# Performance work log

Measured on AMD Instinct MI355X. Metric: run time of the kernel, lower is better.

## Reference

```python
import jax, jax.numpy as jnp
import numpy as np

B, V, L, D, H, W = 4, 2, 8192, 768, 12, 512  # batch, views, seq, d_model, heads, window


def _layernorm(x, g, b, eps=1e-5):
    # matches torch LayerNorm computed in fp32 then cast back
    x32 = x.astype(jnp.float32)
    m = x32.mean(-1, keepdims=True)
    v = ((x32 - m) ** 2).mean(-1, keepdims=True)
    return ((x32 - m) * jax.lax.rsqrt(v + eps) * g + b).astype(x.dtype)


def _mha(q_in, k_in, v_in, wqkv, bqkv, wo, bo, h):
    # torch nn.MultiheadAttention (eval mode, no mask). inputs [..., S, d]
    d = q_in.shape[-1]
    hd = d // h
    scale = 1.0 / np.sqrt(hd)
    q = (q_in @ wqkv[:d].T + bqkv[:d]).reshape(*q_in.shape[:-1], h, hd)
    k = (k_in @ wqkv[d:2 * d].T + bqkv[d:2 * d]).reshape(*k_in.shape[:-1], h, hd)
    v = (v_in @ wqkv[2 * d:].T + bqkv[2 * d:]).reshape(*v_in.shape[:-1], h, hd)
    scores = jnp.einsum('...qhd,...khd->...hqk', q, k) * scale
    a = jax.nn.softmax(scores, axis=-1)
    o = jnp.einsum('...hqk,...khd->...qhd', a, v).reshape(q_in.shape)
    return o @ wo.T + bo


def reference(x, ln1_g, ln1_b, ln2_g, ln2_b,
              a1_wqkv, a1_bqkv, a1_wo, a1_bo,
              a2_wqkv, a2_bqkv, a2_wo, a2_bo,
              fc_w, fc_b, proj_w, proj_b, index):
    b, v, l, c = x.shape
    y = _layernorm(x, ln1_g, ln1_b)
    shifted = (index % 2 == 1)  # index is a static Python int
    xs = jnp.roll(x, W // 2, axis=2) if shifted else x
    p = l // W
    xw = xs.reshape(b, v, p, W, c)  # window partition (only x is rolled, as in source)
    yw = y.reshape(b, v, p, W, c)
    # cross-view windowed attention: Q=norm view i, K=norm view j, V=raw view i
    v1 = _mha(yw[:, 0], yw[:, 1], xw[:, 0], a1_wqkv, a1_bqkv, a1_wo, a1_bo, H)
    v2 = _mha(yw[:, 1], yw[:, 0], xw[:, 1], a2_wqkv, a2_bqkv, a2_wo, a2_bo, H)
    att = jnp.stack([v1, v2], axis=1).reshape(b, v, l, c)
    if shifted:
        att = jnp.roll(att, -(W // 2), axis=2)
    x = x + att
    y2 = _layernorm(x, ln2_g, ln2_b)
    h = y2 @ fc_w.T + fc_b
    h = h * jax.nn.sigmoid(1.702 * h)  # fast GELU
    return x + (h @ proj_w.T + proj_b)


def setup_inputs() -> dict:
    key = jax.random.key(0)
    ks = jax.random.split(key, 10)
    s = 0.02
    return {
        'x': jax.random.normal(ks[0], (B, V, L, D), jnp.float32),
        'ln1_g': jnp.ones((D,), jnp.float32),
        'ln1_b': jnp.zeros((D,), jnp.float32),
        'ln2_g': jnp.ones((D,), jnp.float32),
        'ln2_b': jnp.zeros((D,), jnp.float32),
        'a1_wqkv': jax.random.normal(ks[1], (3 * D, D), jnp.float32) * s,
        'a1_bqkv': jnp.zeros((3 * D,), jnp.float32),
        'a1_wo': jax.random.normal(ks[2], (D, D), jnp.float32) * s,
        'a1_bo': jnp.zeros((D,), jnp.float32),
        'a2_wqkv': jax.random.normal(ks[3], (3 * D, D), jnp.float32) * s,
        'a2_bqkv': jnp.zeros((3 * D,), jnp.float32),
        'a2_wo': jax.random.normal(ks[4], (D, D), jnp.float32) * s,
        'a2_bo': jnp.zeros((D,), jnp.float32),
        'fc_w': jax.random.normal(ks[5], (4 * D, D), jnp.float32) * s,
        'fc_b': jnp.zeros((4 * D,), jnp.float32),
        'proj_w': jax.random.normal(ks[6], (D, 4 * D), jnp.float32) * s,
        'proj_b': jnp.zeros((D,), jnp.float32),
        'index': 0,
    }
```

## Files before the change

kernel.cpp:

```cpp
#include <hip/hip_runtime.h>
#include <hip/hip_bf16.h>

typedef __bf16 bf16x8 __attribute__((ext_vector_type(8)));
typedef float  f32x4  __attribute__((ext_vector_type(4)));
typedef short  s16x4  __attribute__((ext_vector_type(4)));
typedef unsigned short u16;

#define L2E 1.44269504088896f
#define SBAR  __builtin_amdgcn_s_barrier()
#define SCHED __builtin_amdgcn_sched_barrier(0)

static __device__ __forceinline__ u16 f2bf(float f) {
  unsigned u = __builtin_bit_cast(unsigned, f);
  u += 0x7fffu + ((u >> 16) & 1u);
  return (u16)(u >> 16);
}

static __device__ __forceinline__ void gld_lds16(const void* g, void* l) {
  __builtin_amdgcn_global_load_lds((const __attribute__((address_space(1))) unsigned*)g,
                                   (__attribute__((address_space(3))) unsigned*)l, 16, 0, 0);
}

__global__ __launch_bounds__(256)
void cvtk(const float* __restrict__ s, u16* __restrict__ d, int n) {
  const int i = (blockIdx.x * 256 + threadIdx.x) * 4;
  if (i >= n) return;
  const float4 f = *(const float4*)(s + i);
  s16x4 p;
  p[0] = (short)f2bf(f.x); p[1] = (short)f2bf(f.y);
  p[2] = (short)f2bf(f.z); p[3] = (short)f2bf(f.w);
  *(s16x4*)(d + i) = p;
}

__global__ __launch_bounds__(256)
void lnk(const float* __restrict__ x, const float* __restrict__ gw,
         const float* __restrict__ bw, u16* __restrict__ y,
         u16* __restrict__ xv, int viewmajor) {
  const int lane = threadIdx.x & 63;
  const int tok = blockIdx.x * 4 + (threadIdx.x >> 6);
  const float* xr = x + (size_t)tok * 768;
  float4 v[3];
  float s = 0.f, sq = 0.f;
#pragma unroll
  for (int j = 0; j < 3; ++j) {
    v[j] = *(const float4*)(xr + j * 256 + lane * 4);
    s  += v[j].x + v[j].y + v[j].z + v[j].w;
    sq += v[j].x * v[j].x + v[j].y * v[j].y + v[j].z * v[j].z + v[j].w * v[j].w;
  }
#pragma unroll
  for (int o = 1; o < 64; o <<= 1) { s += __shfl_xor(s, o); sq += __shfl_xor(sq, o); }
  const float mean = s * (1.f / 768.f);
  const float var  = sq * (1.f / 768.f) - mean * mean;
  const float rstd = rsqrtf(var + 1e-5f);
  size_t yrow = (size_t)tok;
  if (viewmajor) {
    const int b_ = tok >> 14, vv = (tok >> 13) & 1, l_ = tok & 8191;
    yrow = ((size_t)((vv << 2) + b_) << 13) + l_;
  }
#pragma unroll
  for (int j = 0; j < 3; ++j) {
    const float4 g4 = *(const float4*)(gw + j * 256 + lane * 4);
    const float4 b4 = *(const float4*)(bw + j * 256 + lane * 4);
    s16x4 py;
    py[0] = (short)f2bf((v[j].x - mean) * rstd * g4.x + b4.x);
    py[1] = (short)f2bf((v[j].y - mean) * rstd * g4.y + b4.y);
    py[2] = (short)f2bf((v[j].z - mean) * rstd * g4.z + b4.z);
    py[3] = (short)f2bf((v[j].w - mean) * rstd * g4.w + b4.w);
    *(s16x4*)(y + yrow * 768 + j * 256 + lane * 4) = py;
    if (xv) {
      s16x4 px;
      px[0] = (short)f2bf(v[j].x); px[1] = (short)f2bf(v[j].y);
      px[2] = (short)f2bf(v[j].z); px[3] = (short)f2bf(v[j].w);
      *(s16x4*)(xv + yrow * 768 + j * 256 + lane * 4) = px;
    }
  }
}

template<int MODE>
__global__ __launch_bounds__(512, 2)
void gemm_bt(const u16* __restrict__ A, const u16* __restrict__ B,
             const float* __restrict__ bias, void* __restrict__ Cp,
             int N, int K,
             const float* __restrict__ xres, const int* __restrict__ idxp,
             int vview) {
  __shared__ char lds[131072];
  const int t = threadIdx.x;
  const int lane = t & 63;
  const int wid = t >> 6;
  const int wm = wid >> 2, wn = wid & 3;

  const int cpx = gridDim.x >> 3;
  const int bid = (blockIdx.x & 7) * cpx + (blockIdx.x >> 3);
  const int Ntiles = N >> 8;
  const int PPB = Ntiles << 3;
  const int panel = bid / PPB;
  const int rem = bid - panel * PPB;
  const int nt = rem >> 3;
  const int mt = (panel << 3) + (rem & 7);

  const int urow = t >> 3;
  const int koff = ((t & 7) ^ (urow & 7)) << 3;
  const u16* Asrc = A + (size_t)(mt * 256 + urow) * K + koff;
  const u16* Bsrc = B + (size_t)(nt * 256 + urow) * K + koff;
  const int wdst = wid << 10;

  auto stgA = [&](int d, int kt, int u0) {
    char* base = (char*)lds + d * 32768 + wdst;
    gld_lds16(Asrc + (size_t)(u0 * 64) * K + kt * 64, base + u0 * 8192);
    gld_lds16(Asrc + (size_t)(u0 * 64 + 64) * K + kt * 64, base + u0 * 8192 + 8192);
  };
  auto stgB = [&](int d, int kt, int u0) {
    char* base = (char*)lds + 65536 + d * 32768 + wdst;
    gld_lds16(Bsrc + (size_t)(u0 * 64) * K + kt * 64, base + u0 * 8192);
    gld_lds16(Bsrc + (size_t)(u0 * 64 + 64) * K + kt * 64, base + u0 * 8192 + 8192);
  };

  const int c15 = lane & 15, g = lane >> 4;
  const int axor = c15 & 7;
  const char* LAb = (char*)lds + (wm * 128 + c15) * 128;
  const char* LBb = (char*)lds + 65536 + (wn * 64 + c15) * 128;
  bf16x8 av[4][2], bv[4][2];
  auto rdA = [&](int d, int mh) {
#pragma unroll
    for (int m = 0; m < 4; ++m)
#pragma unroll
      for (int ks = 0; ks < 2; ++ks)
        av[m][ks] = *(const bf16x8*)(LAb + d * 32768 + (mh * 64 + m * 16) * 128 +
                                     (((ks << 2) | g) ^ axor) * 16);
  };
  auto rdB = [&](int d) {
#pragma unroll
    for (int n = 0; n < 4; ++n)
#pragma unroll
      for (int ks = 0; ks < 2; ++ks)
        bv[n][ks] = *(const bf16x8*)(LBb + d * 32768 + (n * 16) * 128 +
                                     (((ks << 2) | g) ^ axor) * 16);
  };

  f32x4 acc[8][4] = {};
  auto QD = [&](int mh, int nh) {
    __builtin_amdgcn_s_setprio(1);
#pragma unroll
    for (int ks = 0; ks < 2; ++ks)
#pragma unroll
      for (int m = 0; m < 4; ++m)
#pragma unroll
        for (int n = 0; n < 2; ++n)
          acc[mh * 4 + m][nh * 2 + n] = __builtin_amdgcn_mfma_f32_16x16x32_bf16(
              av[m][ks], bv[nh * 2 + n][ks], acc[mh * 4 + m][nh * 2 + n], 0, 0, 0);
    __builtin_amdgcn_s_setprio(0);
  };

  const int nk = K >> 6, niter = nk >> 1, last = nk - 1;

  stgA(0, 0, 0); stgA(0, 0, 2); stgB(0, 0, 0); stgB(0, 0, 2);
  stgB(1, 1, 0); stgB(1, 1, 2); stgA(1, 1, 0);
  asm volatile("s_waitcnt vmcnt(6)" ::: "memory");
  SBAR; SCHED;

  for (int it = 0; it < niter; ++it) {
    const int i2 = it * 2;
    const int t1 = (i2 + 1 < nk) ? i2 + 1 : last;
    const int t2 = (i2 + 2 < nk) ? i2 + 2 : last;
    const int t3 = (i2 + 3 < nk) ? i2 + 3 : last;

    rdA(0, 0); rdB(0); stgA(1, t1, 2);
    SCHED; SBAR; SCHED; QD(0, 0); SCHED; SBAR; SCHED;
    stgB(0, t2, 0);
    SCHED; SBAR; SCHED; QD(0, 1); SCHED; SBAR; SCHED;
    rdA(0, 1); stgB(0, t2, 2);
    SCHED; SBAR; SCHED; QD(1, 1); SCHED; SBAR; SCHED;
    stgA(0, t2, 0);
    asm volatile("s_waitcnt vmcnt(6)" ::: "memory");
    SCHED; SBAR; SCHED; QD(1, 0); SCHED; SBAR; SCHED;
    rdA(1, 0); rdB(1); stgA(0, t2, 2);
    SCHED; SBAR; SCHED; QD(0, 0); SCHED; SBAR; SCHED;
    stgB(1, t3, 0);
    SCHED; SBAR; SCHED; QD(0, 1); SCHED; SBAR; SCHED;
    rdA(1, 1); stgB(1, t3, 2);
    SCHED; SBAR; SCHED; QD(1, 1); SCHED; SBAR; SCHED;
    stgA(1, t3, 0);
    asm volatile("s_waitcnt vmcnt(6)" ::: "memory");
    SCHED; SBAR; SCHED; QD(1, 0); SCHED; SBAR; SCHED;
  }

  int shift = 0;
  if constexpr (MODE == 2) shift = (idxp[0] & 1) ? 256 : 0;

  const int rb0 = mt * 256 + wm * 128 + (g << 2);
  const int cbase = nt * 256 + wn * 64 + c15;
#pragma unroll
  for (int mi = 0; mi < 8; ++mi) {
    const int row = rb0 + mi * 16;
#pragma unroll
    for (int nj = 0; nj < 4; ++nj) {
      const int col = cbase + nj * 16;
      const float bvv = bias[col];
      if constexpr (MODE == 0) {
        u16* C = (u16*)Cp;
#pragma unroll
        for (int r = 0; r < 4; ++r)
          C[(size_t)(row + r) * N + col] = f2bf(acc[mi][nj][r] + bvv);
      } else if constexpr (MODE == 1) {
        u16* C = (u16*)Cp;
        const int hh = col >> 6, dd = col & 63;
        const int b_ = row >> 13, l_ = row & 8191;
        s16x4 pk;
#pragma unroll
        for (int r = 0; r < 4; ++r) pk[r] = (short)f2bf(acc[mi][nj][r] + bvv);
        *(s16x4*)(C + (((size_t)((b_ * 12 + hh) << 6) + dd) << 13) + l_) = pk;
      } else if constexpr (MODE == 2) {
        float* C = (float*)Cp;
        const int b_ = row >> 13, p_ = row & 8191;
        const int l0 = (p_ - shift) & 8191;
        const size_t rbase = ((size_t)((b_ << 1) + vview) << 13) + l0;
#pragma unroll
        for (int r = 0; r < 4; ++r) {
          const size_t idx = (rbase + r) * 768 + col;
          C[idx] = xres[idx] + acc[mi][nj][r] + bvv;
        }
      } else if constexpr (MODE == 3) {
        u16* C = (u16*)Cp;
#pragma unroll
        for (int r = 0; r < 4; ++r) {
          const float u = acc[mi][nj][r] + bvv;
          const float e = __builtin_amdgcn_exp2f(-2.45546693f * u);
          C[(size_t)(row + r) * N + col] = f2bf(u / (1.f + e));
        }
      } else {
        float* C = (float*)Cp;
#pragma unroll
        for (int r = 0; r < 4; ++r) {
          const size_t idx = (size_t)(row + r) * 768 + col;
          C[idx] = C[idx] + acc[mi][nj][r] + bvv;
        }
      }
    }
  }
}

__global__ __launch_bounds__(512, 2)
void attnk(const u16* __restrict__ Q1, const u16* __restrict__ K1, const u16* __restrict__ V1,
           const u16* __restrict__ Q2, const u16* __restrict__ K2, const u16* __restrict__ V2,
           u16* __restrict__ O, const int* __restrict__ idxp) {
  __shared__ char lds[131072];
  const int t = threadIdx.x;
  const int lane = t & 63;
  const int c = lane & 15, g = lane >> 4;
  const int wid = t >> 6;
  int bb = blockIdx.x;
  const int h = bb % 12; bb /= 12;
  const int w = bb & 15; bb >>= 4;
  const int b = bb & 3;
  const int a = bb >> 2;
  const int shift = (idxp[0] & 1) ? 256 : 0;

  const u16* Q  = a ? Q2 : Q1;
  const u16* Kb = a ? K2 : K1;
  const u16* Vt = a ? V2 : V1;
  const int kbase = b * 8192 + w * 512;
  const u16* Vts = Vt + ((size_t)(b * 12 + h) << 19);

  const int qrow0 = b * 8192 + w * 512 + wid * 64;
  bf16x8 qf[4][2];
#pragma unroll
  for (int q = 0; q < 4; ++q)
#pragma unroll
    for (int hf = 0; hf < 2; ++hf)
      qf[q][hf] = *(const bf16x8*)(Q + (size_t)(qrow0 + q * 16 + c) * 768 + h * 64 + hf * 32 + g * 8);

  {
    const int r0 = t >> 3, ch = t & 7;
    char* kdst = (char*)lds + (wid << 10);
#pragma unroll
    for (int p = 0; p < 8; ++p) {
      const int row = p * 64 + r0;
      gld_lds16(Kb + (size_t)(kbase + row) * 768 + h * 64 + ((ch ^ (row & 7)) << 3),
                kdst + p * 8192);
    }
    char* vdst = (char*)lds + 65536 + (wid << 10);
#pragma unroll
    for (int p = 0; p < 8; ++p) {
      const int vrow = p * 8 + wid;
      const int cg = lane ^ (vrow & 7);
      const int l = (w * 512 + cg * 8 - shift) & 8191;
      gld_lds16(Vts + (size_t)vrow * 8192 + l, vdst + p * 8192);
    }
  }
  __syncthreads();

  f32x4 oacc[4][4] = {};
  f32x4 psum[4] = {};
  const float CEXP = 0.125f * L2E;
  const char* LK = (char*)lds;
  const char* LV = (char*)lds + 65536;

  for (int kt = 0; kt < 32; ++kt) {
    const int krow = kt * 16 + c;
    const int ksw = krow & 7;
    const bf16x8 kf0 = *(const bf16x8*)(LK + krow * 128 + ((g ^ ksw) << 4));
    const bf16x8 kf1 = *(const bf16x8*)(LK + krow * 128 + (((4 | g) ^ ksw) << 4));
    s16x4 vf[4];
#pragma unroll
    for (int df = 0; df < 4; ++df) {
      const int vr = df * 16 + c;
      vf[df] = *(const s16x4*)(LV + vr * 1024 +
                               (((kt * 2 + (g >> 1)) ^ (vr & 7)) << 4) + ((g & 1) << 3));
    }

    const f32x4 z = {0.f, 0.f, 0.f, 0.f};
    s16x4 pk[4];
#pragma unroll
    for (int q = 0; q < 4; ++q) {
      f32x4 sc2 = __builtin_amdgcn_mfma_f32_16x16x32_bf16(kf0, qf[q][0], z, 0, 0, 0);
      sc2 = __builtin_amdgcn_mfma_f32_16x16x32_bf16(kf1, qf[q][1], sc2, 0, 0, 0);
      f32x4 pv;
      pv[0] = __builtin_amdgcn_exp2f(sc2[0] * CEXP);
      pv[1] = __builtin_amdgcn_exp2f(sc2[1] * CEXP);
      pv[2] = __builtin_amdgcn_exp2f(sc2[2] * CEXP);
      pv[3] = __builtin_amdgcn_exp2f(sc2[3] * CEXP);
      psum[q] += pv;
      pk[q][0] = (short)f2bf(pv[0]);
      pk[q][1] = (short)f2bf(pv[1]);
      pk[q][2] = (short)f2bf(pv[2]);
      pk[q][3] = (short)f2bf(pv[3]);
    }
#pragma unroll
    for (int df = 0; df < 4; ++df)
#pragma unroll
      for (int q = 0; q < 4; ++q)
        oacc[df][q] = __builtin_amdgcn_mfma_f32_16x16x16bf16_1k(vf[df], pk[q], oacc[df][q], 0, 0, 0);
  }

  const size_t orow0 = (size_t)(a * 32768 + qrow0);
#pragma unroll
  for (int q = 0; q < 4; ++q) {
    float ss = psum[q][0] + psum[q][1] + psum[q][2] + psum[q][3];
    ss += __shfl_xor(ss, 16);
    ss += __shfl_xor(ss, 32);
    const float inv = 1.f / ss;
#pragma unroll
    for (int df = 0; df < 4; ++df) {
      s16x4 po;
#pragma unroll
      for (int r = 0; r < 4; ++r) po[r] = (short)f2bf(oacc[df][q][r] * inv);
      *(s16x4*)(O + (orow0 + q * 16 + c) * 768 + h * 64 + df * 16 + g * 4) = po;
    }
  }
}

extern "C" void kernel_launch(void* const* d_in, const int* in_sizes, int n_in,
                              void* d_out, int out_size, void* d_ws, size_t ws_size,
                              hipStream_t stream) {
  const float* x       = (const float*)d_in[0];
  const float* ln1_g   = (const float*)d_in[1];
  const float* ln1_b   = (const float*)d_in[2];
  const float* ln2_g   = (const float*)d_in[3];
  const float* ln2_b   = (const float*)d_in[4];
  const float* a1_wqkv = (const float*)d_in[5];
  const float* a1_bqkv = (const float*)d_in[6];
  const float* a1_wo   = (const float*)d_in[7];
  const float* a1_bo   = (const float*)d_in[8];
  const float* a2_wqkv = (const float*)d_in[9];
  const float* a2_bqkv = (const float*)d_in[10];
  const float* a2_wo   = (const float*)d_in[11];
  const float* a2_bo   = (const float*)d_in[12];
  const float* fc_w    = (const float*)d_in[13];
  const float* fc_b    = (const float*)d_in[14];
  const float* proj_w  = (const float*)d_in[15];
  const float* proj_b  = (const float*)d_in[16];
  const int*   idxp    = (const int*)d_in[17];
  float* out = (float*)d_out;

  u16* p = (u16*)d_ws;
  u16* w1  = p; p += (size_t)2304 * 768;
  u16* w2  = p; p += (size_t)2304 * 768;
  u16* wo1 = p; p += (size_t)768 * 768;
  u16* wo2 = p; p += (size_t)768 * 768;
  u16* fcw = p; p += (size_t)3072 * 768;
  u16* pjw = p; p += (size_t)768 * 3072;
  u16* y   = p; p += (size_t)65536 * 768;
  u16* xv  = p; p += (size_t)65536 * 768;
  u16* Q1  = p; p += (size_t)32768 * 768;
  u16* K1  = p; p += (size_t)32768 * 768;
  u16* V1  = p; p += (size_t)32768 * 768;
  u16* Q2  = p; p += (size_t)32768 * 768;
  u16* K2  = p; p += (size_t)32768 * 768;
  u16* V2  = p; p += (size_t)32768 * 768;
  u16* Ob  = p; p += (size_t)65536 * 768;
  u16* hb  = Q1;

  cvtk<<<1728, 256, 0, stream>>>(a1_wqkv, w1, 2304 * 768);
  cvtk<<<1728, 256, 0, stream>>>(a2_wqkv, w2, 2304 * 768);
  cvtk<<<576,  256, 0, stream>>>(a1_wo, wo1, 768 * 768);
  cvtk<<<576,  256, 0, stream>>>(a2_wo, wo2, 768 * 768);
  cvtk<<<2304, 256, 0, stream>>>(fc_w, fcw, 3072 * 768);
  cvtk<<<2304, 256, 0, stream>>>(proj_w, pjw, 768 * 3072);

  lnk<<<16384, 256, 0, stream>>>(x, ln1_g, ln1_b, y, xv, 1);

  const size_t VS = (size_t)32768 * 768;
  gemm_bt<0><<<384, 512, 0, stream>>>(y,        w1,                  a1_bqkv,        Q1, 768, 768, nullptr, nullptr, 0);
  gemm_bt<0><<<384, 512, 0, stream>>>(y + VS,   w1 + 768 * 768,      a1_bqkv + 768,  K1, 768, 768, nullptr, nullptr, 0);
  gemm_bt<1><<<384, 512, 0, stream>>>(xv,       w1 + 2 * 768 * 768,  a1_bqkv + 1536, V1, 768, 768, nullptr, nullptr, 0);
  gemm_bt<0><<<384, 512, 0, stream>>>(y + VS,   w2,                  a2_bqkv,        Q2, 768, 768, nullptr, nullptr, 0);
  gemm_bt<0><<<384, 512, 0, stream>>>(y,        w2 + 768 * 768,      a2_bqkv + 768,  K2, 768, 768, nullptr, nullptr, 0);
  gemm_bt<1><<<384, 512, 0, stream>>>(xv + VS,  w2 + 2 * 768 * 768,  a2_bqkv + 1536, V2, 768, 768, nullptr, nullptr, 0);

  attnk<<<1536, 512, 0, stream>>>(Q1, K1, V1, Q2, K2, V2, Ob, idxp);

  gemm_bt<2><<<384, 512, 0, stream>>>(Ob,      wo1, a1_bo, out, 768, 768, x, idxp, 0);
  gemm_bt<2><<<384, 512, 0, stream>>>(Ob + VS, wo2, a2_bo, out, 768, 768, x, idxp, 1);

  lnk<<<16384, 256, 0, stream>>>(out, ln2_g, ln2_b, y, nullptr, 0);

  gemm_bt<3><<<3072, 512, 0, stream>>>(y, fcw, fc_b, hb, 3072, 768, nullptr, nullptr, 0);

  gemm_bt<4><<<768, 512, 0, stream>>>(hb, pjw, proj_b, out, 768, 3072, nullptr, nullptr, 0);
}
```

Measured before the change: 1.502 ms.

## Replace 256x256 8-wave GEMM with 256x128 4-wave grouped GEMM kernel

Replaces the templated 256x256-tile, 512-thread GEMM and its hand-interleaved 8-phase schedule with a 256x128-tile, 256-thread kernel. The new kernel uses a simple double-buffered K=32 loop and a smaller LDS footprint so more blocks can be resident. Several GEMMs are batched into a single grouped launch through an argument struct: the six QKV projections in one, the two output projections in another. The epilogue mode becomes a runtime branch instead of a template parameter. This trades the tuned fine-grained MFMA/load interleaving and larger-tile reuse for fewer launches and higher occupancy, at the cost of more barriers per unit of work.

```diff
diff --git a/kernel.cpp b/kernel.cpp
--- a/kernel.cpp
+++ b/kernel.cpp
@@ -7,7 +7,6 @@
 typedef unsigned short u16;
 
 #define L2E 1.44269504088896f
-#define SBAR  __builtin_amdgcn_s_barrier()
 #define SCHED __builtin_amdgcn_sched_barrier(0)
 
 static __device__ __forceinline__ u16 f2bf(float f) {
@@ -76,119 +75,106 @@
   }
 }
 
-template<int MODE>
-__global__ __launch_bounds__(512, 2)
-void gemm_bt(const u16* __restrict__ A, const u16* __restrict__ B,
-             const float* __restrict__ bias, void* __restrict__ Cp,
-             int N, int K,
-             const float* __restrict__ xres, const int* __restrict__ idxp,
-             int vview) {
-  __shared__ char lds[131072];
+struct GArgs {
+  const u16* A[6]; const u16* B[6]; const float* bias[6]; void* C[6];
+  int mode[6]; int vv[6];
+  int bps, N, K;
+  const float* xres; const int* idxp;
+};
+
+__global__ __launch_bounds__(256, 2)
+void gemmk(GArgs ga) {
+  __shared__ char lds[49152];
   const int t = threadIdx.x;
   const int lane = t & 63;
   const int wid = t >> 6;
-  const int wm = wid >> 2, wn = wid & 3;
-
-  const int cpx = gridDim.x >> 3;
-  const int bid = (blockIdx.x & 7) * cpx + (blockIdx.x >> 3);
-  const int Ntiles = N >> 8;
+  const int wm = wid >> 1, wn = wid & 1;
+
+  const int sub = blockIdx.x / ga.bps;
+  const int local = blockIdx.x - sub * ga.bps;
+  const u16* A = ga.A[sub];
+  const u16* B = ga.B[sub];
+  const float* bias = ga.bias[sub];
+  void* Cp = ga.C[sub];
+  const int mode = ga.mode[sub];
+  const int vview = ga.vv[sub];
+  const int N = ga.N, K = ga.K;
+
+  const int cpx = ga.bps >> 3;
+  const int bid = (local & 7) * cpx + (local >> 3);
+  const int Ntiles = N >> 7;
   const int PPB = Ntiles << 3;
   const int panel = bid / PPB;
   const int rem = bid - panel * PPB;
   const int nt = rem >> 3;
   const int mt = (panel << 3) + (rem & 7);
 
-  const int urow = t >> 3;
-  const int koff = ((t & 7) ^ (urow & 7)) << 3;
-  const u16* Asrc = A + (size_t)(mt * 256 + urow) * K + koff;
-  const u16* Bsrc = B + (size_t)(nt * 256 + urow) * K + koff;
+  const int r0 = t >> 2;
+  const int csrc = (t & 3) ^ ((r0 >> 1) & 3);
+  const u16* Asrc = A + (size_t)(mt * 256 + r0) * K + csrc * 8;
+  const u16* Bsrc = B + (size_t)(nt * 128 + r0) * K + csrc * 8;
   const int wdst = wid << 10;
 
-  auto stgA = [&](int d, int kt, int u0) {
-    char* base = (char*)lds + d * 32768 + wdst;
-    gld_lds16(Asrc + (size_t)(u0 * 64) * K + kt * 64, base + u0 * 8192);
-    gld_lds16(Asrc + (size_t)(u0 * 64 + 64) * K + kt * 64, base + u0 * 8192 + 8192);
+  auto stage = [&](int d, int kt) {
+#pragma unroll
+    for (int i = 0; i < 4; ++i)
+      gld_lds16(Asrc + (size_t)(i * 64) * K + kt * 32,
+                (char*)lds + d * 16384 + i * 4096 + wdst);
+#pragma unroll
+    for (int i = 0; i < 2; ++i)
+      gld_lds16(Bsrc + (size_t)(i * 64) * K + kt * 32,
+                (char*)lds + 32768 + d * 8192 + i * 4096 + wdst);
   };
-  auto stgB = [&](int d, int kt, int u0) {
-    char* base = (char*)lds + 65536 + d * 32768 + wdst;
-    gld_lds16(Bsrc + (size_t)(u0 * 64) * K + kt * 64, base + u0 * 8192);
-    gld_lds16(Bsrc + (size_t)(u0 * 64 + 64) * K + kt * 64, base + u0 * 8192 + 8192);
-  };
 
   const int c15 = lane & 15, g = lane >> 4;
-  const int axor = c15 & 7;
-  const char* LAb = (char*)lds + (wm * 128 + c15) * 128;
-  const char* LBb = (char*)lds + 65536 + (wn * 64 + c15) * 128;
-  bf16x8 av[4][2], bv[4][2];
-  auto rdA = [&](int d, int mh) {
-#pragma unroll
-    for (int m = 0; m < 4; ++m)
-#pragma unroll
-      for (int ks = 0; ks < 2; ++ks)
-        av[m][ks] = *(const bf16x8*)(LAb + d * 32768 + (mh * 64 + m * 16) * 128 +
-                                     (((ks << 2) | g) ^ axor) * 16);
+  bf16x8 av[8], bv[4];
+  auto rdA = [&](int d) {
+#pragma unroll
+    for (int m = 0; m < 8; ++m) {
+      const int row = wm * 128 + m * 16 + c15;
+      av[m] = *(const bf16x8*)((char*)lds + d * 16384 + row * 64 +
+                               ((g ^ ((row >> 1) & 3)) << 4));
+    }
   };
   auto rdB = [&](int d) {
 #pragma unroll
-    for (int n = 0; n < 4; ++n)
-#pragma unroll
-      for (int ks = 0; ks < 2; ++ks)
-        bv[n][ks] = *(const bf16x8*)(LBb + d * 32768 + (n * 16) * 128 +
-                                     (((ks << 2) | g) ^ axor) * 16);
+    for (int n = 0; n < 4; ++n) {
+      const int row = wn * 64 + n * 16 + c15;
+      bv[n] = *(const bf16x8*)((char*)lds + 32768 + d * 8192 + row * 64 +
+                               ((g ^ ((row >> 1) & 3)) << 4));
+    }
   };
 
   f32x4 acc[8][4] = {};
-  auto QD = [&](int mh, int nh) {
+  const int nk = K >> 5;
+
+  stage(0, 0);
+#pragma unroll 2
+  for (int kt = 0; kt < nk; ++kt) {
+    const int d = kt & 1;
+    if (kt + 1 < nk) {
+      stage(d ^ 1, kt + 1);
+      asm volatile("s_waitcnt vmcnt(6)" ::: "memory");
+    } else {
+      asm volatile("s_waitcnt vmcnt(0)" ::: "memory");
+    }
+    __builtin_amdgcn_s_barrier();
+    SCHED;
+    rdA(d); rdB(d);
     __builtin_amdgcn_s_setprio(1);
 #pragma unroll
-    for (int ks = 0; ks < 2; ++ks)
-#pragma unroll
-      for (int m = 0; m < 4; ++m)
-#pragma unroll
-        for (int n = 0; n < 2; ++n)
-          acc[mh * 4 + m][nh * 2 + n] = __builtin_amdgcn_mfma_f32_16x16x32_bf16(
-              av[m][ks], bv[nh * 2 + n][ks], acc[mh * 4 + m][nh * 2 + n], 0, 0, 0);
+    for (int m = 0; m < 8; ++m)
+#pragma unroll
+      for (int n = 0; n < 4; ++n)
+        acc[m][n] = __builtin_amdgcn_mfma_f32_16x16x32_bf16(av[m], bv[n], acc[m][n], 0, 0, 0);
     __builtin_amdgcn_s_setprio(0);
-  };
-
-  const int nk = K >> 6, niter = nk >> 1, last = nk - 1;
-
-  stgA(0, 0, 0); stgA(0, 0, 2); stgB(0, 0, 0); stgB(0, 0, 2);
-  stgB(1, 1, 0); stgB(1, 1, 2); stgA(1, 1, 0);
-  asm volatile("s_waitcnt vmcnt(6)" ::: "memory");
-  SBAR; SCHED;
-
-  for (int it = 0; it < niter; ++it) {
-    const int i2 = it * 2;
-    const int t1 = (i2 + 1 < nk) ? i2 + 1 : last;
-    const int t2 = (i2 + 2 < nk) ? i2 + 2 : last;
-    const int t3 = (i2 + 3 < nk) ? i2 + 3 : last;
-
-    rdA(0, 0); rdB(0); stgA(1, t1, 2);
-    SCHED; SBAR; SCHED; QD(0, 0); SCHED; SBAR; SCHED;
-    stgB(0, t2, 0);
-    SCHED; SBAR; SCHED; QD(0, 1); SCHED; SBAR; SCHED;
-    rdA(0, 1); stgB(0, t2, 2);
-    SCHED; SBAR; SCHED; QD(1, 1); SCHED; SBAR; SCHED;
-    stgA(0, t2, 0);
-    asm volatile("s_waitcnt vmcnt(6)" ::: "memory");
-    SCHED; SBAR; SCHED; QD(1, 0); SCHED; SBAR; SCHED;
-    rdA(1, 0); rdB(1); stgA(0, t2, 2);
-    SCHED; SBAR; SCHED; QD(0, 0); SCHED; SBAR; SCHED;
-    stgB(1, t3, 0);
-    SCHED; SBAR; SCHED; QD(0, 1); SCHED; SBAR; SCHED;
-    rdA(1, 1); stgB(1, t3, 2);
-    SCHED; SBAR; SCHED; QD(1, 1); SCHED; SBAR; SCHED;
-    stgA(1, t3, 0);
-    asm volatile("s_waitcnt vmcnt(6)" ::: "memory");
-    SCHED; SBAR; SCHED; QD(1, 0); SCHED; SBAR; SCHED;
-  }
-
-  int shift = 0;
-  if constexpr (MODE == 2) shift = (idxp[0] & 1) ? 256 : 0;
-
+    SCHED;
+    __builtin_amdgcn_s_barrier();
+  }
+
+  const int shift = (mode == 2 && (ga.idxp[0] & 1)) ? 256 : 0;
   const int rb0 = mt * 256 + wm * 128 + (g << 2);
-  const int cbase = nt * 256 + wn * 64 + c15;
+  const int cbase = nt * 128 + wn * 64 + c15;
 #pragma unroll
   for (int mi = 0; mi < 8; ++mi) {
     const int row = rb0 + mi * 16;
@@ -196,12 +182,12 @@
     for (int nj = 0; nj < 4; ++nj) {
       const int col = cbase + nj * 16;
       const float bvv = bias[col];
-      if constexpr (MODE == 0) {
+      if (mode == 0) {
         u16* C = (u16*)Cp;
 #pragma unroll
         for (int r = 0; r < 4; ++r)
           C[(size_t)(row + r) * N + col] = f2bf(acc[mi][nj][r] + bvv);
-      } else if constexpr (MODE == 1) {
+      } else if (mode == 1) {
         u16* C = (u16*)Cp;
         const int hh = col >> 6, dd = col & 63;
         const int b_ = row >> 13, l_ = row & 8191;
@@ -209,7 +195,7 @@
 #pragma unroll
         for (int r = 0; r < 4; ++r) pk[r] = (short)f2bf(acc[mi][nj][r] + bvv);
         *(s16x4*)(C + (((size_t)((b_ * 12 + hh) << 6) + dd) << 13) + l_) = pk;
-      } else if constexpr (MODE == 2) {
+      } else if (mode == 2) {
         float* C = (float*)Cp;
         const int b_ = row >> 13, p_ = row & 8191;
         const int l0 = (p_ - shift) & 8191;
@@ -217,9 +203,9 @@
 #pragma unroll
         for (int r = 0; r < 4; ++r) {
           const size_t idx = (rbase + r) * 768 + col;
-          C[idx] = xres[idx] + acc[mi][nj][r] + bvv;
+          C[idx] = ga.xres[idx] + acc[mi][nj][r] + bvv;
         }
-      } else if constexpr (MODE == 3) {
+      } else if (mode == 3) {
         u16* C = (u16*)Cp;
 #pragma unroll
         for (int r = 0; r < 4; ++r) {
@@ -400,21 +386,42 @@
   lnk<<<16384, 256, 0, stream>>>(x, ln1_g, ln1_b, y, xv, 1);
 
   const size_t VS = (size_t)32768 * 768;
-  gemm_bt<0><<<384, 512, 0, stream>>>(y,        w1,                  a1_bqkv,        Q1, 768, 768, nullptr, nullptr, 0);
-  gemm_bt<0><<<384, 512, 0, stream>>>(y + VS,   w1 + 768 * 768,      a1_bqkv + 768,  K1, 768, 768, nullptr, nullptr, 0);
-  gemm_bt<1><<<384, 512, 0, stream>>>(xv,       w1 + 2 * 768 * 768,  a1_bqkv + 1536, V1, 768, 768, nullptr, nullptr, 0);
-  gemm_bt<0><<<384, 512, 0, stream>>>(y + VS,   w2,                  a2_bqkv,        Q2, 768, 768, nullptr, nullptr, 0);
-  gemm_bt<0><<<384, 512, 0, stream>>>(y,        w2 + 768 * 768,      a2_bqkv + 768,  K2, 768, 768, nullptr, nullptr, 0);
-  gemm_bt<1><<<384, 512, 0, stream>>>(xv + VS,  w2 + 2 * 768 * 768,  a2_bqkv + 1536, V2, 768, 768, nullptr, nullptr, 0);
+
+  {
+    GArgs ga = {};
+    ga.A[0] = y;       ga.B[0] = w1;                 ga.bias[0] = a1_bqkv;        ga.C[0] = Q1; ga.mode[0] = 0;
+    ga.A[1] = y + VS;  ga.B[1] = w1 + 768 * 768;     ga.bias[1] = a1_bqkv + 768;  ga.C[1] = K1; ga.mode[1] = 0;
+    ga.A[2] = xv;      ga.B[2] = w1 + 2 * 768 * 768; ga.bias[2] = a1_bqkv + 1536; ga.C[2] = V1; ga.mode[2] = 1;
+    ga.A[3] = y + VS;  ga.B[3] = w2;                 ga.bias[3] = a2_bqkv;        ga.C[3] = Q2; ga.mode[3] = 0;
+    ga.A[4] = y;       ga.B[4] = w2 + 768 * 768;     ga.bias[4] = a2_bqkv + 768;  ga.C[4] = K2; ga.mode[4] = 0;
+    ga.A[5] = xv + VS; ga.B[5] = w2 + 2 * 768 * 768; ga.bias[5] = a2_bqkv + 1536; ga.C[5] = V2; ga.mode[5] = 1;
+    ga.bps = 768; ga.N = 768; ga.K = 768; ga.xres = nullptr; ga.idxp = idxp;
+    gemmk<<<4608, 256, 0, stream>>>(ga);
+  }
 
   attnk<<<1536, 512, 0, stream>>>(Q1, K1, V1, Q2, K2, V2, Ob, idxp);
 
-  gemm_bt<2><<<384, 512, 0, stream>>>(Ob,      wo1, a1_bo, out, 768, 768, x, idxp, 0);
-  gemm_bt<2><<<384, 512, 0, stream>>>(Ob + VS, wo2, a2_bo, out, 768, 768, x, idxp, 1);
+  {
+    GArgs ga = {};
+    ga.A[0] = Ob;      ga.B[0] = wo1; ga.bias[0] = a1_bo; ga.C[0] = out; ga.mode[0] = 2; ga.vv[0] = 0;
+    ga.A[1] = Ob + VS; ga.B[1] = wo2; ga.bias[1] = a2_bo; ga.C[1] = out; ga.mode[1] = 2; ga.vv[1] = 1;
+    ga.bps = 768; ga.N = 768; ga.K = 768; ga.xres = x; ga.idxp = idxp;
+    gemmk<<<1536, 256, 0, stream>>>(ga);
+  }
 
   lnk<<<16384, 256, 0, stream>>>(out, ln2_g, ln2_b, y, nullptr, 0);
 
-  gemm_bt<3><<<3072, 512, 0, stream>>>(y, fcw, fc_b, hb, 3072, 768, nullptr, nullptr, 0);
-
-  gemm_bt<4><<<768, 512, 0, stream>>>(hb, pjw, proj_b, out, 768, 3072, nullptr, nullptr, 0);
-}
+  {
+    GArgs ga = {};
+    ga.A[0] = y; ga.B[0] = fcw; ga.bias[0] = fc_b; ga.C[0] = hb; ga.mode[0] = 3;
+    ga.bps = 6144; ga.N = 3072; ga.K = 768; ga.xres = nullptr; ga.idxp = idxp;
+    gemmk<<<6144, 256, 0, stream>>>(ga);
+  }
+
+  {
+    GArgs ga = {};
+    ga.A[0] = hb; ga.B[0] = pjw; ga.bias[0] = proj_b; ga.C[0] = out; ga.mode[0] = 4;
+    ga.bps = 1536; ga.N = 768; ga.K = 3072; ga.xres = nullptr; ga.idxp = idxp;
+    gemmk<<<1536, 256, 0, stream>>>(ga);
+  }
+}
```

New measurement: 1.798 ms. +19.7%, slower.
